# Optimization experiments

Hardware: AMD Instinct MI355X
Metric: run time of the kernel (lower is better)

Reference implementation:

```python
import jax, jax.numpy as jnp
import numpy as np

B, S, D, K = 128, 200, 128, 4
NQ, NC = 10000, 500


def setup_inputs() -> dict:
    key = jax.random.key(0)
    ks = jax.random.split(key, 20)
    f = jnp.float32
    inp = {}
    inp["question_seq"] = jax.random.randint(ks[0], (B, S), 0, NQ)
    inp["hint_attempt_seq"] = jax.random.randint(ks[1], (B, S), 0, 12)
    inp["correct_seq"] = jax.random.randint(ks[2], (B, S), 0, 2)
    inp["interval_time_seq"] = jax.random.randint(ks[3], (B, S), 0, 100)
    inp["use_time_seq"] = jax.random.randint(ks[4], (B, S), 0, 100)
    inp["q2c_table"] = jax.random.randint(ks[5], (NQ, K), 0, NC)
    inp["q2c_mask_table"] = jax.random.randint(ks[6], (NQ, K), 0, 2)
    s = 0.1
    inp["embed_question"] = jax.random.normal(ks[7], (NQ, D), f) * s
    inp["embed_question_disc"] = jax.random.normal(ks[8], (NQ, 1), f) * s
    inp["embed_concept"] = jax.random.normal(ks[9], (NC, D), f) * s
    inp["embed_interval_time"] = jax.random.normal(ks[10], (100, D), f) * s
    inp["embed_use_time"] = jax.random.normal(ks[11], (100, D), f) * s
    inp["embed_hint_attempt"] = jax.random.normal(ks[12], (12, D), f) * s
    inp["W_fuse"] = jax.random.normal(ks[13], (2 * D, D), f) / np.float32(np.sqrt(2 * D))
    inp["b_fuse"] = jnp.zeros((D,), f)
    inp["W_absorb"] = jax.random.normal(ks[14], (3 * D, D), f) / np.float32(np.sqrt(3 * D))
    inp["b_absorb"] = jnp.zeros((D,), f)
    inp["W_forget"] = jax.random.normal(ks[15], (3 * D, D), f) / np.float32(np.sqrt(3 * D))
    inp["b_forget"] = jnp.zeros((D,), f)
    inp["latent0"] = jax.random.normal(ks[16], (B, D), f) * 0.1  # xavier-init latent_pre
    return inp


def _cos(a, b, eps=1e-8):
    # torch.cosine_similarity semantics with eps clamp on each norm
    num = jnp.sum(a * b, axis=-1)
    na = jnp.sqrt(jnp.sum(a * a, axis=-1))
    nb = jnp.sqrt(jnp.sum(b * b, axis=-1))
    return num / (jnp.maximum(na, eps) * jnp.maximum(nb, eps))


def _forward(question_seq, hint_attempt_seq, correct_seq, interval_time_seq, use_time_seq,
             q2c_table, q2c_mask_table,
             embed_question, embed_question_disc, embed_concept, embed_interval_time,
             embed_use_time, embed_hint_attempt,
             W_fuse, b_fuse, W_absorb, b_absorb, W_forget, b_forget, latent0):
    f = latent0.dtype
    qe = embed_question[question_seq]                                # [B,S,D]
    qd = jax.nn.sigmoid(embed_question_disc[question_seq]) * 10.0    # [B,S,1]
    ce = jnp.broadcast_to(correct_seq.astype(f)[:, :, None], qe.shape)  # [B,S,D]
    ite = embed_interval_time[interval_time_seq]                     # [B,S,D]
    ute = embed_use_time[use_time_seq]                               # [B,S,D]
    hae = embed_hint_attempt[hint_attempt_seq]                       # [B,S,D]
    cp = embed_concept[q2c_table[question_seq]]                      # [B,S,K,D]
    m = q2c_mask_table[question_seq].astype(f)                       # [B,S,K]

    tm = lambda x: jnp.swapaxes(x, 0, 1)  # time-major for scan
    xs = (tm(qe[:, :-1]), tm(ce[:, :-1]), tm(ute[:, :-1]), tm(hae[:, :-1]), tm(ite[:, :-1]),
          tm(cp[:, :-1]), tm(cp[:, 1:]), tm(qd[:, 1:]), tm(m[:, :-1]))

    def step(lp, x):
        qe_t, ce_t, ute_t, hae_t, ite_t, cp_t, cp_t1, qd_t1, m_t = x
        inter = jnp.concatenate([qe_t, ce_t], axis=-1) @ W_fuse + b_fuse
        absorb = jnp.concatenate([inter, ute_t, hae_t], axis=-1) @ W_absorb + b_absorb
        forget = jax.nn.sigmoid(jnp.concatenate([lp, ite_t, inter], axis=-1) @ W_forget + b_forget)
        lc = lp * forget + absorb  # dropout p=0 -> identity
        qdiff = (_cos(qe_t[:, None, :], cp_t) + 1.0) * 0.5   # [B,K]
        uab = (_cos(lc[:, None, :], cp_t1) + 1.0) * 0.5      # [B,K]
        logit = qd_t1[:, 0] * jnp.sum((uab - qdiff) * m_t, axis=-1)  # [B]
        return lc, jax.nn.sigmoid(logit)

    _, ys = jax.lax.scan(step, latent0, xs)  # ys: [S-1, B]
    y = jnp.concatenate([ys.T, jnp.zeros((latent0.shape[0], 1), f)], axis=1)  # [B,S], last col 0
    return y


def reference(question_seq, hint_attempt_seq, correct_seq, interval_time_seq, use_time_seq,
              q2c_table, q2c_mask_table,
              embed_question, embed_question_disc, embed_concept, embed_interval_time,
              embed_use_time, embed_hint_attempt,
              W_fuse, b_fuse, W_absorb, b_absorb, W_forget, b_forget, latent0):
    return _forward(question_seq, hint_attempt_seq, correct_seq, interval_time_seq, use_time_seq,
                    q2c_table, q2c_mask_table,
                    embed_question, embed_question_disc, embed_concept, embed_interval_time,
                    embed_use_time, embed_hint_attempt,
                    W_fuse, b_fuse, W_absorb, b_absorb, W_forget, b_forget, latent0)
```

## Files before the change

kernel.cpp:

```cpp
#include <hip/hip_runtime.h>
#include <hip/hip_bf16.h>

typedef unsigned short u16;

#define Bb  128
#define Ss  200
#define Tt  199
#define Dd  128
#define Kk  4
#define NQq 10000
#define NCc 500
#define CHK 16
#define NCH 13

__device__ inline float bf2f(u16 u) {
    union { unsigned int i; float f; } x;
    x.i = ((unsigned int)u) << 16;
    return x.f;
}

__device__ inline float ldf(const void* p, int i, int m) {
    if (m) return ((const float*)p)[i];
    return bf2f(((const u16*)p)[i]);
}

__device__ inline void stf(void* p, int i, int m, float v) {
    if (m) ((float*)p)[i] = v;
    else ((__hip_bfloat16*)p)[i] = __float2bfloat16(v);
}

__device__ inline int clampi(int v, int lo, int hi) {
    return v < lo ? lo : (v > hi ? hi : v);
}

__device__ inline float wave_red(float v) {
#pragma unroll
    for (int m = 32; m >= 1; m >>= 1) v += __shfl_xor(v, m);
    return v;
}

__device__ inline float4 f4add(float4 a, float4 b) {
    return make_float4(a.x + b.x, a.y + b.y, a.z + b.z, a.w + b.w);
}
__device__ inline float4 f4fma(float s, float4 a, float4 b) {
    return make_float4(fmaf(s, a.x, b.x), fmaf(s, a.y, b.y),
                       fmaf(s, a.z, b.z), fmaf(s, a.w, b.w));
}

__device__ inline int detect_mode(const void* Eq) {
    const u16* q = (const u16*)Eq;
    const int l = threadIdx.x & 63;
    float mx = 0.f;
#pragma unroll
    for (int k = 0; k < 4; ++k) {
        float a = fabsf(bf2f(q[l * 4 + k]));
        if (!(a == a)) a = 3.0e38f;
        mx = fmaxf(mx, a);
    }
#pragma unroll
    for (int s = 32; s >= 1; s >>= 1) mx = fmaxf(mx, __shfl_xor(mx, s));
    return (mx > 1.0e6f) ? 1 : 0;
}

__global__ __launch_bounds__(128) void k_prep(
    const void* Eq, const void* Wf, const void* Wa, const void* Wg,
    const void* bfu, const void* ba, const void* bg,
    const void* Eut, const void* Eha, const void* Eit, const void* Ec,
    float* cnorm, float* BabT, float* BfgT,
    float* vA0, float* vA1, float* vF0, float* vF1,
    float* PA_ut, float* PA_ha, float* PF_it) {
    const int m = detect_mode(Eq);
    const int bi = blockIdx.x, tid = threadIdx.x;
    __shared__ float cs2s[128];
    __shared__ float tmp[2];
    if (bi < 500) {
        const int c = bi;
        float v = ldf(Ec, c * 128 + tid, m);
        float s = wave_red(v * v);
        if ((tid & 63) == 0) tmp[tid >> 6] = s;
        __syncthreads();
        if (tid == 0) cnorm[c] = fmaxf(sqrtf(tmp[0] + tmp[1]), 1e-8f);
    } else if (bi < 628) {
        const int r = bi - 500;
        float acc = 0.f;
        for (int j = 0; j < 128; ++j)
            acc += ldf(Wf, r * 128 + j, m) * ldf(Wa, j * 128 + tid, m);
        BabT[r * 128 + tid] = acc;
    } else if (bi < 756) {
        const int r = bi - 628;
        float acc = 0.f;
        for (int j = 0; j < 128; ++j)
            acc += ldf(Wf, r * 128 + j, m) * ldf(Wg, (256 + j) * 128 + tid, m);
        BfgT[r * 128 + tid] = acc;
    } else if (bi == 756) {
        float s = 0.f;
        for (int r = 0; r < 128; ++r) s += ldf(Wf, (128 + r) * 128 + tid, m);
        cs2s[tid] = s;
        __syncthreads();
        float a0 = 0.f, a1 = 0.f;
        for (int j = 0; j < 128; ++j) {
            float wv = ldf(Wa, j * 128 + tid, m);
            a0 += ldf(bfu, j, m) * wv;
            a1 += cs2s[j] * wv;
        }
        vA0[tid] = a0 + ldf(ba, tid, m);
        vA1[tid] = a1;
    } else if (bi == 757) {
        float s = 0.f;
        for (int r = 0; r < 128; ++r) s += ldf(Wf, (128 + r) * 128 + tid, m);
        cs2s[tid] = s;
        __syncthreads();
        float a0 = 0.f, a1 = 0.f;
        for (int j = 0; j < 128; ++j) {
            float wv = ldf(Wg, (256 + j) * 128 + tid, m);
            a0 += ldf(bfu, j, m) * wv;
            a1 += cs2s[j] * wv;
        }
        vF0[tid] = a0 + ldf(bg, tid, m);
        vF1[tid] = a1;
    } else if (bi < 858) {
        const int r = bi - 758;
        float acc = 0.f;
        for (int j = 0; j < 128; ++j)
            acc += ldf(Eut, r * 128 + j, m) * ldf(Wa, (128 + j) * 128 + tid, m);
        PA_ut[r * 128 + tid] = acc;
    } else if (bi < 870) {
        const int r = bi - 858;
        float acc = 0.f;
        for (int j = 0; j < 128; ++j)
            acc += ldf(Eha, r * 128 + j, m) * ldf(Wa, (256 + j) * 128 + tid, m);
        PA_ha[r * 128 + tid] = acc;
    } else {
        const int r = bi - 870;
        float acc = 0.f;
        for (int j = 0; j < 128; ++j)
            acc += ldf(Eit, r * 128 + j, m) * ldf(Wg, (128 + j) * 128 + tid, m);
        PF_it[r * 128 + tid] = acc;
    }
}

__global__ __launch_bounds__(256) void k_mid(
    const void* Eq, const void* Eqd, const void* Ec,
    const int* q2c, const int* q2cm,
    const float* BabT, const float* BfgT, const float* cnorm,
    float* PA_q, float* PF_q, float* qdm, float* qd10) {
    const int m = detect_mode(Eq);
    const int tid = threadIdx.x;
    const int bi = blockIdx.x;
    if (bi < 313) {
        __shared__ float At[32][36];
        __shared__ float Bt0[32][128];
        __shared__ float Bt1[32][128];
        const int r0 = bi * 32;
        float acc0[2][8], acc1[2][8];
#pragma unroll
        for (int j = 0; j < 2; ++j)
#pragma unroll
            for (int i = 0; i < 8; ++i) { acc0[j][i] = 0.f; acc1[j][i] = 0.f; }
        const int tx = tid & 15, ty = tid >> 4;
        for (int ks = 0; ks < 4; ++ks) {
            {
                const int row = tid >> 3, seg = tid & 7;
                const int q = clampi(r0 + row, 0, NQq - 1);
                const int ei = q * 128 + ks * 32 + seg * 4;
                float* dst = &At[row][seg * 4];
                if (m) {
                    float4 v = *(const float4*)((const float*)Eq + ei);
                    dst[0] = v.x; dst[1] = v.y; dst[2] = v.z; dst[3] = v.w;
                } else {
                    uint2 v = *(const uint2*)((const u16*)Eq + ei);
                    dst[0] = bf2f((u16)(v.x & 0xffff)); dst[1] = bf2f((u16)(v.x >> 16));
                    dst[2] = bf2f((u16)(v.y & 0xffff)); dst[3] = bf2f((u16)(v.y >> 16));
                }
            }
            {
                const float4* s0 = (const float4*)(BabT + ks * 32 * 128);
                const float4* s1 = (const float4*)(BfgT + ks * 32 * 128);
                float4* d0 = (float4*)&Bt0[0][0];
                float4* d1 = (float4*)&Bt1[0][0];
#pragma unroll
                for (int k = 0; k < 4; ++k) {
                    d0[tid + k * 256] = s0[tid + k * 256];
                    d1[tid + k * 256] = s1[tid + k * 256];
                }
            }
            __syncthreads();
#pragma unroll
            for (int kk = 0; kk < 32; kk += 4) {
                float a_[2][4];
                *(float4*)&a_[0][0] = *(const float4*)&At[ty * 2 + 0][kk];
                *(float4*)&a_[1][0] = *(const float4*)&At[ty * 2 + 1][kk];
#pragma unroll
                for (int q = 0; q < 4; ++q) {
                    float4 b0 = *(const float4*)&Bt0[kk + q][tx * 8];
                    float4 b1 = *(const float4*)&Bt0[kk + q][tx * 8 + 4];
                    float4 c0 = *(const float4*)&Bt1[kk + q][tx * 8];
                    float4 c1 = *(const float4*)&Bt1[kk + q][tx * 8 + 4];
#pragma unroll
                    for (int j = 0; j < 2; ++j) {
                        const float av = a_[j][q];
                        acc0[j][0] += av * b0.x; acc0[j][1] += av * b0.y;
                        acc0[j][2] += av * b0.z; acc0[j][3] += av * b0.w;
                        acc0[j][4] += av * b1.x; acc0[j][5] += av * b1.y;
                        acc0[j][6] += av * b1.z; acc0[j][7] += av * b1.w;
                        acc1[j][0] += av * c0.x; acc1[j][1] += av * c0.y;
                        acc1[j][2] += av * c0.z; acc1[j][3] += av * c0.w;
                        acc1[j][4] += av * c1.x; acc1[j][5] += av * c1.y;
                        acc1[j][6] += av * c1.z; acc1[j][7] += av * c1.w;
                    }
                }
            }
            __syncthreads();
        }
#pragma unroll
        for (int j = 0; j < 2; ++j) {
            const int q = r0 + ty * 2 + j;
            if (q < NQq) {
                float* oa = PA_q + q * 128 + tx * 8;
                float* of = PF_q + q * 128 + tx * 8;
#pragma unroll
                for (int i = 0; i < 8; ++i) { oa[i] = acc0[j][i]; of[i] = acc1[j][i]; }
            }
        }
    } else {
        const int wv = tid >> 6, lane = tid & 63;
        const int q = (bi - 313) * 4 + wv;
        const float qa = ldf(Eq, q * 128 + lane, m);
        const float qb = ldf(Eq, q * 128 + 64 + lane, m);
        const float nqc = fmaxf(sqrtf(wave_red(qa * qa + qb * qb)), 1e-8f);
        const int4 cc = ((const int4*)q2c)[q];
        const int4 mm = ((const int4*)q2cm)[q];
        const int cks[4] = {clampi(cc.x, 0, NCc - 1), clampi(cc.y, 0, NCc - 1),
                            clampi(cc.z, 0, NCc - 1), clampi(cc.w, 0, NCc - 1)};
        const int ms[4]  = {mm.x, mm.y, mm.z, mm.w};
        float qs = 0.f;
#pragma unroll
        for (int k = 0; k < 4; ++k) {
            const int ck = cks[k];
            float dot = wave_red(qa * ldf(Ec, ck * 128 + lane, m) +
                                 qb * ldf(Ec, ck * 128 + 64 + lane, m));
            qs += (float)ms[k] * (0.5f * dot / (nqc * cnorm[ck]) + 0.5f);
        }
        if (lane == 0) {
            qdm[q] = qs;
            qd10[q] = 10.f / (1.f + __expf(-ldf(Eqd, q, m)));
        }
    }
}

__global__ __launch_bounds__(256) void p4_scan(
    const int* q_seq, const int* ut_seq, const int* ha_seq, const int* it_seq,
    const int* c_seq,
    const void* Eq, const void* Wg, const void* L0,
    const float* PA_q, const float* PA_ut, const float* PA_ha,
    const float* PF_q, const float* PF_it,
    const float* vA0, const float* vA1, const float* vF0, const float* vF1,
    float* lc_seq) {
    const int m = detect_mode(Eq);
    const int b = blockIdx.x;
    const int tid = threadIdx.x;
    const int wv = tid >> 6, l = tid & 63;
    const int d0 = 2 * l;
    const int ib = wv << 5;
    const int dd = ib + (l & 31);

    __shared__ float part[2][4][128];
    __shared__ float st_ab[CHK * 128];
    __shared__ float st_pf[CHK * 128];

    float wA[32], wB[32];
#pragma unroll
    for (int k = 0; k < 32; ++k) {
        wA[k] = ldf(Wg, (ib + k) * 128 + d0, m);
        wB[k] = ldf(Wg, (ib + k) * 128 + d0 + 1, m);
    }
    float lc = (l < 32) ? ldf(L0, b * 128 + dd, m) : 0.f;

    const int srow = tid >> 4, seg = tid & 15;
    const int off8 = seg * 8;
    const float4 A0a = *(const float4*)(vA0 + off8), A0b = *(const float4*)(vA0 + off8 + 4);
    const float4 A1a = *(const float4*)(vA1 + off8), A1b = *(const float4*)(vA1 + off8 + 4);
    const float4 F0a = *(const float4*)(vF0 + off8), F0b = *(const float4*)(vF0 + off8 + 4);
    const float4 F1a = *(const float4*)(vF1 + off8), F1b = *(const float4*)(vF1 + off8 + 4);

    float4 qa0, qa1, ua0, ua1, ga0, ga1, qf0, qf1, if0, if1;
    float cf;
#define LOAD_CHUNK(C)                                                          \
    {                                                                          \
        int tt = (C) * CHK + srow; if (tt > Tt - 1) tt = Tt - 1;               \
        const int base = b * Ss + tt;                                          \
        const int qt = clampi(q_seq[base], 0, NQq - 1);                        \
        const int ut = clampi(ut_seq[base], 0, 99);                            \
        const int ha = clampi(ha_seq[base], 0, 11);                            \
        const int it = clampi(it_seq[base], 0, 99);                            \
        cf = (float)c_seq[base];                                               \
        const float* pq = PA_q + qt * 128 + off8;                              \
        qa0 = *(const float4*)pq; qa1 = *(const float4*)(pq + 4);              \
        const float* pu = PA_ut + ut * 128 + off8;                             \
        ua0 = *(const float4*)pu; ua1 = *(const float4*)(pu + 4);              \
        const float* ph = PA_ha + ha * 128 + off8;                             \
        ga0 = *(const float4*)ph; ga1 = *(const float4*)(ph + 4);              \
        const float* pf = PF_q + qt * 128 + off8;                              \
        qf0 = *(const float4*)pf; qf1 = *(const float4*)(pf + 4);              \
        const float* pi = PF_it + it * 128 + off8;                             \
        if0 = *(const float4*)pi; if1 = *(const float4*)(pi + 4);              \
    }

    LOAD_CHUNK(0)
    float lcbuf[CHK];
    int par = 0;

    for (int c = 0; c < NCH; ++c) {
        __syncthreads();
        {
            float4 ab0 = f4fma(cf, A1a, f4add(f4add(qa0, ua0), f4add(ga0, A0a)));
            float4 ab1 = f4fma(cf, A1b, f4add(f4add(qa1, ua1), f4add(ga1, A0b)));
            float4 pf0 = f4fma(cf, F1a, f4add(qf0, f4add(if0, F0a)));
            float4 pf1 = f4fma(cf, F1b, f4add(qf1, f4add(if1, F0b)));
            float4* sa = (float4*)(st_ab + srow * 128 + off8);
            sa[0] = ab0; sa[1] = ab1;
            float4* sp = (float4*)(st_pf + srow * 128 + off8);
            sp[0] = pf0; sp[1] = pf1;
        }
        if (c + 1 < NCH) LOAD_CHUNK(c + 1)
        __syncthreads();

#pragma unroll
        for (int s = 0; s < CHK; ++s) {
            float pa = 0.f, pb = 0.f;
#pragma unroll
            for (int k = 0; k < 32; ++k) {
                const float u = __uint_as_float(
                    __builtin_amdgcn_readlane(__float_as_uint(lc), k));
                pa = fmaf(u, wA[k], pa);
                pb = fmaf(u, wB[k], pb);
            }
            *(float2*)&part[par][wv][d0] = make_float2(pa, pb);
            __syncthreads();
            if (l < 32) {
                const float fs = part[par][0][dd] + part[par][1][dd]
                               + part[par][2][dd] + part[par][3][dd];
                const float ab = st_ab[(s << 7) + dd];
                const float pf = st_pf[(s << 7) + dd];
                const float fg = 1.f / (1.f + __expf(-(fs + pf)));
                lc = lc * fg + ab;
                lcbuf[s] = lc;
            }
            par ^= 1;
        }
        if (l < 32) {
#pragma unroll
            for (int s = 0; s < CHK; ++s) {
                const int t = c * CHK + s;
                if (t < Tt)
                    lc_seq[((long)t * 128 + b) * 128 + dd] = lcbuf[s];
            }
        }
    }
#undef LOAD_CHUNK
}

__global__ __launch_bounds__(256) void p5_out(
    const int* q_seq, const int* q2c, const int* q2cm,
    const float* lc_seq, const float* qdm, const float* qd10,
    const float* cnorm, const void* Eq, const void* Ec, void* out) {
    const int m = detect_mode(Eq);
    const int wv = threadIdx.x >> 6, lane = threadIdx.x & 63;
    const int r = blockIdx.x * 4 + wv;
    const int t = r >> 7, b = r & 127;
    const int qt  = clampi(q_seq[b * Ss + t], 0, NQq - 1);
    const int qt1 = clampi(q_seq[b * Ss + t + 1], 0, NQq - 1);
    const int4 mm = ((const int4*)q2cm)[qt];
    int4 ci = ((const int4*)q2c)[qt1];
    const int c0 = clampi(ci.x, 0, NCc - 1), c1 = clampi(ci.y, 0, NCc - 1);
    const int c2 = clampi(ci.z, 0, NCc - 1), c3 = clampi(ci.w, 0, NCc - 1);
    const float la = lc_seq[(long)r * 128 + lane];
    const float lb = lc_seq[(long)r * 128 + 64 + lane];
    float nl = la * la + lb * lb;
    float d0 = la * ldf(Ec, c0 * 128 + lane, m) + lb * ldf(Ec, c0 * 128 + 64 + lane, m);
    float d1 = la * ldf(Ec, c1 * 128 + lane, m) + lb * ldf(Ec, c1 * 128 + 64 + lane, m);
    float d2 = la * ldf(Ec, c2 * 128 + lane, m) + lb * ldf(Ec, c2 * 128 + 64 + lane, m);
    float d3 = la * ldf(Ec, c3 * 128 + lane, m) + lb * ldf(Ec, c3 * 128 + 64 + lane, m);
#pragma unroll
    for (int s = 32; s >= 1; s >>= 1) {
        nl += __shfl_xor(nl, s);
        d0 += __shfl_xor(d0, s); d1 += __shfl_xor(d1, s);
        d2 += __shfl_xor(d2, s); d3 += __shfl_xor(d3, s);
    }
    if (lane == 0) {
        const float inl = 1.f / fmaxf(sqrtf(nl), 1e-8f);
        const float accv = (float)mm.x * (0.5f * d0 * inl / cnorm[c0] + 0.5f)
                         + (float)mm.y * (0.5f * d1 * inl / cnorm[c1] + 0.5f)
                         + (float)mm.z * (0.5f * d2 * inl / cnorm[c2] + 0.5f)
                         + (float)mm.w * (0.5f * d3 * inl / cnorm[c3] + 0.5f);
        const float logit = qd10[qt1] * (accv - qdm[qt]);
        stf(out, b * Ss + t, m, 1.f / (1.f + __expf(-logit)));
        if (t == 0) stf(out, b * Ss + 199, m, 0.f);
    }
}

extern "C" void kernel_launch(void* const* d_in, const int* in_sizes, int n_in,
                              void* d_out, int out_size, void* d_ws, size_t ws_size,
                              hipStream_t stream) {
    (void)in_sizes; (void)n_in; (void)out_size; (void)ws_size;
    const int* q_seq  = (const int*)d_in[0];
    const int* ha_seq = (const int*)d_in[1];
    const int* c_seq  = (const int*)d_in[2];
    const int* it_seq = (const int*)d_in[3];
    const int* ut_seq = (const int*)d_in[4];
    const int* q2c    = (const int*)d_in[5];
    const int* q2cm   = (const int*)d_in[6];
    const void* Eq   = d_in[7];
    const void* Eqd  = d_in[8];
    const void* Ec   = d_in[9];
    const void* Eit  = d_in[10];
    const void* Eut  = d_in[11];
    const void* Eha  = d_in[12];
    const void* Wf   = d_in[13];
    const void* bfu  = d_in[14];
    const void* Wa   = d_in[15];
    const void* ba   = d_in[16];
    const void* Wg   = d_in[17];
    const void* bg   = d_in[18];
    const void* L0   = d_in[19];

    float* cnorm = (float*)d_ws;
    float* vA0   = cnorm + 512;
    float* vA1   = vA0 + 128;
    float* vF0   = vA1 + 128;
    float* vF1   = vF0 + 128;
    float* BabT  = vF1 + 128;
    float* BfgT  = BabT + 16384;
    float* PA_ut = BfgT + 16384;
    float* PA_ha = PA_ut + 12800;
    float* PF_it = PA_ha + 1536;
    float* qdm   = PF_it + 12800;
    float* qd10  = qdm + 10016;
    float* PA_q  = qd10 + 10016;
    float* PF_q  = PA_q + 1280000;
    float* lc_seq= PF_q + 1280000;

    hipLaunchKernelGGL(k_prep, dim3(970), dim3(128), 0, stream,
                       Eq, Wf, Wa, Wg, bfu, ba, bg, Eut, Eha, Eit, Ec,
                       cnorm, BabT, BfgT, vA0, vA1, vF0, vF1, PA_ut, PA_ha, PF_it);
    hipLaunchKernelGGL(k_mid, dim3(2813), dim3(256), 0, stream,
                       Eq, Eqd, Ec, q2c, q2cm, BabT, BfgT, cnorm,
                       PA_q, PF_q, qdm, qd10);
    hipLaunchKernelGGL(p4_scan, dim3(Bb), dim3(256), 0, stream,
                       q_seq, ut_seq, ha_seq, it_seq, c_seq, Eq, Wg, L0,
                       PA_q, PA_ut, PA_ha, PF_q, PF_it,
                       vA0, vA1, vF0, vF1, lc_seq);
    hipLaunchKernelGGL(p5_out, dim3(Tt * Bb / 4), dim3(256), 0, stream,
                       q_seq, q2c, q2cm, lc_seq, qdm, qd10, cnorm, Eq, Ec, d_out);
}
```

Baseline: 235.4 us.

## Process two batch rows per block in the recurrent scan kernel

The sequential scan kernel now handles two independent batch chains per block, interleaving their matvec and gate updates. Each chain step has a serial barrier plus a readlane/FMA latency chain. Running two chains lets those latencies overlap and halves the number of barriers per batch row, while the register-resident weights are shared. The cost is fewer blocks (64 on a GPU with many more CUs), higher register pressure, and a longer per-step critical path. This kernel is likely the dominant stage of the pipeline.

```diff
diff --git a/kernel.cpp b/kernel.cpp
--- a/kernel.cpp
+++ b/kernel.cpp
@@ -257,16 +257,16 @@
     const float* vA0, const float* vA1, const float* vF0, const float* vF1,
     float* lc_seq) {
     const int m = detect_mode(Eq);
-    const int b = blockIdx.x;
+    const int b0 = blockIdx.x * 2;
     const int tid = threadIdx.x;
     const int wv = tid >> 6, l = tid & 63;
     const int d0 = 2 * l;
     const int ib = wv << 5;
     const int dd = ib + (l & 31);
 
-    __shared__ float part[2][4][128];
-    __shared__ float st_ab[CHK * 128];
-    __shared__ float st_pf[CHK * 128];
+    __shared__ float part[2][2][4][128];
+    __shared__ float st_ab[2][CHK * 128];
+    __shared__ float st_pf[2][CHK * 128];
 
     float wA[32], wB[32];
 #pragma unroll
@@ -274,7 +274,10 @@
         wA[k] = ldf(Wg, (ib + k) * 128 + d0, m);
         wB[k] = ldf(Wg, (ib + k) * 128 + d0 + 1, m);
     }
-    float lc = (l < 32) ? ldf(L0, b * 128 + dd, m) : 0.f;
+    float lc[2];
+#pragma unroll
+    for (int ch = 0; ch < 2; ++ch)
+        lc[ch] = (l < 32) ? ldf(L0, (b0 + ch) * 128 + dd, m) : 0.f;
 
     const int srow = tid >> 4, seg = tid & 15;
     const int off8 = seg * 8;
@@ -283,68 +286,79 @@
     const float4 F0a = *(const float4*)(vF0 + off8), F0b = *(const float4*)(vF0 + off8 + 4);
     const float4 F1a = *(const float4*)(vF1 + off8), F1b = *(const float4*)(vF1 + off8 + 4);
 
-    float4 qa0, qa1, ua0, ua1, ga0, ga1, qf0, qf1, if0, if1;
-    float cf;
-#define LOAD_CHUNK(C)                                                          \
+    float4 qa0[2], qa1[2], ua0[2], ua1[2], ga0[2], ga1[2];
+    float4 qf0[2], qf1[2], if0[2], if1[2];
+    float cf[2];
+#define LOAD_CHUNK(C, CH)                                                      \
     {                                                                          \
         int tt = (C) * CHK + srow; if (tt > Tt - 1) tt = Tt - 1;               \
-        const int base = b * Ss + tt;                                          \
+        const int base = (b0 + (CH)) * Ss + tt;                                \
         const int qt = clampi(q_seq[base], 0, NQq - 1);                        \
         const int ut = clampi(ut_seq[base], 0, 99);                            \
         const int ha = clampi(ha_seq[base], 0, 11);                            \
         const int it = clampi(it_seq[base], 0, 99);                            \
-        cf = (float)c_seq[base];                                               \
+        cf[CH] = (float)c_seq[base];                                           \
         const float* pq = PA_q + qt * 128 + off8;                              \
-        qa0 = *(const float4*)pq; qa1 = *(const float4*)(pq + 4);              \
+        qa0[CH] = *(const float4*)pq; qa1[CH] = *(const float4*)(pq + 4);      \
         const float* pu = PA_ut + ut * 128 + off8;                             \
-        ua0 = *(const float4*)pu; ua1 = *(const float4*)(pu + 4);              \
+        ua0[CH] = *(const float4*)pu; ua1[CH] = *(const float4*)(pu + 4);      \
         const float* ph = PA_ha + ha * 128 + off8;                             \
-        ga0 = *(const float4*)ph; ga1 = *(const float4*)(ph + 4);              \
+        ga0[CH] = *(const float4*)ph; ga1[CH] = *(const float4*)(ph + 4);      \
         const float* pf = PF_q + qt * 128 + off8;                              \
-        qf0 = *(const float4*)pf; qf1 = *(const float4*)(pf + 4);              \
+        qf0[CH] = *(const float4*)pf; qf1[CH] = *(const float4*)(pf + 4);      \
         const float* pi = PF_it + it * 128 + off8;                             \
-        if0 = *(const float4*)pi; if1 = *(const float4*)(pi + 4);              \
-    }
-
-    LOAD_CHUNK(0)
-    float lcbuf[CHK];
-    int par = 0;
+        if0[CH] = *(const float4*)pi; if1[CH] = *(const float4*)(pi + 4);      \
+    }
+
+    LOAD_CHUNK(0, 0)
+    LOAD_CHUNK(0, 1)
+    float lcbuf[2][CHK];
 
     for (int c = 0; c < NCH; ++c) {
         __syncthreads();
-        {
-            float4 ab0 = f4fma(cf, A1a, f4add(f4add(qa0, ua0), f4add(ga0, A0a)));
-            float4 ab1 = f4fma(cf, A1b, f4add(f4add(qa1, ua1), f4add(ga1, A0b)));
-            float4 pf0 = f4fma(cf, F1a, f4add(qf0, f4add(if0, F0a)));
-            float4 pf1 = f4fma(cf, F1b, f4add(qf1, f4add(if1, F0b)));
-            float4* sa = (float4*)(st_ab + srow * 128 + off8);
+#pragma unroll
+        for (int ch = 0; ch < 2; ++ch) {
+            float4 ab0 = f4fma(cf[ch], A1a,
+                               f4add(f4add(qa0[ch], ua0[ch]), f4add(ga0[ch], A0a)));
+            float4 ab1 = f4fma(cf[ch], A1b,
+                               f4add(f4add(qa1[ch], ua1[ch]), f4add(ga1[ch], A0b)));
+            float4 pf0 = f4fma(cf[ch], F1a, f4add(qf0[ch], f4add(if0[ch], F0a)));
+            float4 pf1 = f4fma(cf[ch], F1b, f4add(qf1[ch], f4add(if1[ch], F0b)));
+            float4* sa = (float4*)(st_ab[ch] + srow * 128 + off8);
             sa[0] = ab0; sa[1] = ab1;
-            float4* sp = (float4*)(st_pf + srow * 128 + off8);
+            float4* sp = (float4*)(st_pf[ch] + srow * 128 + off8);
             sp[0] = pf0; sp[1] = pf1;
         }
-        if (c + 1 < NCH) LOAD_CHUNK(c + 1)
+        if (c + 1 < NCH) { LOAD_CHUNK(c + 1, 0) LOAD_CHUNK(c + 1, 1) }
         __syncthreads();
 
+        int par = 0;
 #pragma unroll
         for (int s = 0; s < CHK; ++s) {
-            float pa = 0.f, pb = 0.f;
-#pragma unroll
-            for (int k = 0; k < 32; ++k) {
-                const float u = __uint_as_float(
-                    __builtin_amdgcn_readlane(__float_as_uint(lc), k));
-                pa = fmaf(u, wA[k], pa);
-                pb = fmaf(u, wB[k], pb);
-            }
-            *(float2*)&part[par][wv][d0] = make_float2(pa, pb);
+#pragma unroll
+            for (int ch = 0; ch < 2; ++ch) {
+                float pa = 0.f, pb = 0.f;
+#pragma unroll
+                for (int k = 0; k < 32; ++k) {
+                    const float u = __uint_as_float(
+                        __builtin_amdgcn_readlane(__float_as_uint(lc[ch]), k));
+                    pa = fmaf(u, wA[k], pa);
+                    pb = fmaf(u, wB[k], pb);
+                }
+                *(float2*)&part[par][ch][wv][d0] = make_float2(pa, pb);
+            }
             __syncthreads();
             if (l < 32) {
-                const float fs = part[par][0][dd] + part[par][1][dd]
-                               + part[par][2][dd] + part[par][3][dd];
-                const float ab = st_ab[(s << 7) + dd];
-                const float pf = st_pf[(s << 7) + dd];
-                const float fg = 1.f / (1.f + __expf(-(fs + pf)));
-                lc = lc * fg + ab;
-                lcbuf[s] = lc;
+#pragma unroll
+                for (int ch = 0; ch < 2; ++ch) {
+                    const float fs = part[par][ch][0][dd] + part[par][ch][1][dd]
+                                   + part[par][ch][2][dd] + part[par][ch][3][dd];
+                    const float ab = st_ab[ch][(s << 7) + dd];
+                    const float pf = st_pf[ch][(s << 7) + dd];
+                    const float fg = 1.f / (1.f + __expf(-(fs + pf)));
+                    lc[ch] = lc[ch] * fg + ab;
+                    lcbuf[ch][s] = lc[ch];
+                }
             }
             par ^= 1;
         }
@@ -352,8 +366,10 @@
 #pragma unroll
             for (int s = 0; s < CHK; ++s) {
                 const int t = c * CHK + s;
-                if (t < Tt)
-                    lc_seq[((long)t * 128 + b) * 128 + dd] = lcbuf[s];
+                if (t < Tt) {
+                    lc_seq[((long)t * 128 + b0) * 128 + dd]     = lcbuf[0][s];
+                    lc_seq[((long)t * 128 + b0 + 1) * 128 + dd] = lcbuf[1][s];
+                }
             }
         }
     }
@@ -446,7 +462,7 @@
     hipLaunchKernelGGL(k_mid, dim3(2813), dim3(256), 0, stream,
                        Eq, Eqd, Ec, q2c, q2cm, BabT, BfgT, cnorm,
                        PA_q, PF_q, qdm, qd10);
-    hipLaunchKernelGGL(p4_scan, dim3(Bb), dim3(256), 0, stream,
+    hipLaunchKernelGGL(p4_scan, dim3(Bb / 2), dim3(256), 0, stream,
                        q_seq, ut_seq, ha_seq, it_seq, c_seq, Eq, Wg, L0,
                        PA_q, PA_ut, PA_ha, PF_q, PF_it,
                        vA0, vA1, vF0, vF1, lc_seq);
```

After: 282.0 us. 19.8% more time.
